# Kernel tuning notes

Measured on AMD Instinct MI355X. Metric: run time of the kernel, lower is better.

The kernel has to match this reference:

```python
import jax, jax.numpy as jnp
import numpy as np

B, S, DIM, H = 2, 2048, 1024, 16
HD = DIM // H  # 64


def setup_inputs() -> dict:
    key = jax.random.key(0)
    ks = jax.random.split(key, 7)
    sc = 1.0 / np.sqrt(DIM)
    gammas = jnp.asarray(1.0 - 2.0 ** (-5.0 - np.arange(H)), jnp.float32)  # RetNet per-head decay
    return {
        "q": jax.random.normal(ks[0], (B, S, DIM), jnp.float32),
        "k": jax.random.normal(ks[1], (B, S, DIM), jnp.float32),
        "v": jax.random.normal(ks[2], (B, S, DIM), jnp.float32),
        "W_in": jax.random.normal(ks[3], (DIM, DIM), jnp.float32) * sc,
        "b_in": jnp.zeros((DIM,), jnp.float32),
        "W_gate": jax.random.normal(ks[4], (DIM, DIM), jnp.float32) * sc,
        "b_gate": jnp.zeros((DIM,), jnp.float32),
        "W_out": jax.random.normal(ks[5], (DIM, DIM), jnp.float32) * sc,
        "b_out": jnp.zeros((DIM,), jnp.float32),
        "gammas": gammas,
    }


def _mamba(x, W_in, b_in, W_gate, b_gate, W_out, b_out):
    # Gated linear recurrence: h_t = a_t * h_{t-1} + u_t  (selective-scan style)
    u = x @ W_in + b_in          # [B,S,D]
    a = jax.nn.sigmoid(x @ W_gate + b_gate)  # [B,S,D] data-dependent decay gate

    def combine(c1, c2):
        a1, u1 = c1
        a2, u2 = c2
        return (a1 * a2, a2 * u1 + u2)

    _, h = jax.lax.associative_scan(combine, (a, u), axis=1)  # parallel scan over S
    return h @ W_out + b_out  # residual=False, dropout=0.0


def _retention(q, k, v, gammas):
    # Per-head decay-masked attention: out = ((Q K^T / sqrt(hd)) * D) V,
    # D[h,n,m] = gamma_h^(n-m) for n>=m else 0 (causal decay kernel).
    def split(x):
        return x.reshape(B, S, H, HD).transpose(0, 2, 1, 3)  # [B,H,S,HD]

    qh, kh, vh = split(q), split(k), split(v)
    idx = jnp.arange(S)
    diff = idx[:, None] - idx[None, :]                        # [S,S]
    expnt = jnp.maximum(diff, 0).astype(jnp.float32)
    D = jnp.where(diff >= 0, gammas[:, None, None] ** expnt, 0.0)  # [H,S,S]
    scores = jnp.einsum("bhnd,bhmd->bhnm", qh, kh) / np.sqrt(HD)
    out = jnp.einsum("bhnm,bhmd->bhnd", scores * D[None], vh)
    return out.transpose(0, 2, 1, 3).reshape(B, S, DIM)


def reference(q, k, v, W_in, b_in, W_gate, b_gate, W_out, b_out, gammas):
    q_proj = _mamba(q, W_in, b_in, W_gate, b_gate, W_out, b_out)
    return _retention(q_proj, k, v, gammas)
```

## Files before the change

kernel.cpp:

```cpp
#include <hip/hip_runtime.h>
#include <math.h>

#define B_  2
#define S_  2048
#define D_  1024
#define H_  16
#define HD_ 64
#define M_  (B_*S_)

typedef unsigned short ushort_t;
typedef unsigned int   uint_t;
typedef __attribute__((ext_vector_type(8))) short bf16x8;
typedef __attribute__((ext_vector_type(4))) float f32x4;

__device__ __forceinline__ ushort_t f2bf(float f) {
    uint_t u = __builtin_bit_cast(uint_t, f);
    u += 0x7FFFu + ((u >> 16) & 1u);
    return (ushort_t)(u >> 16);
}
__device__ __forceinline__ float bf2f(ushort_t h) {
    uint_t u = (uint_t)h << 16;
    return __builtin_bit_cast(float, u);
}
__device__ __forceinline__ uint_t pkt(float lo, float hi) {
    return __builtin_amdgcn_perm(__builtin_bit_cast(uint_t, hi),
                                 __builtin_bit_cast(uint_t, lo), 0x07060302u);
}
__device__ __forceinline__ void dma16(const ushort_t* g, ushort_t* l) {
    __builtin_amdgcn_global_load_lds(
        (const __attribute__((address_space(1))) uint_t*)g,
        (__attribute__((address_space(3))) uint_t*)l, 16, 0, 0);
}
__device__ __forceinline__ bf16x8 fragr(const ushort_t* base, int row, int chunk) {
    return *(const bf16x8*)&base[row * 64 + (((chunk ^ (row & 7)) << 3))];
}

__global__ __launch_bounds__(256)
void prep(const float* __restrict__ W0, const float* __restrict__ W1,
          const float* __restrict__ W2, ushort_t* __restrict__ T0,
          ushort_t* __restrict__ T1, ushort_t* __restrict__ T2,
          const float* __restrict__ X, ushort_t* __restrict__ Y) {
    const int bx = blockIdx.x;
    if (bx >= 3072) {
        const int i = ((bx - 3072) * 256 + threadIdx.x) * 4;
        float4 x = *(const float4*)(X + i);
        *(ushort4*)(Y + i) = make_ushort4(f2bf(x.x), f2bf(x.y), f2bf(x.z), f2bf(x.w));
        return;
    }
    __shared__ float T[32][36];
    const int z = bx >> 10;
    const float*  W  = (z == 0) ? W0 : (z == 1) ? W1 : W2;
    ushort_t*     WT = (z == 0) ? T0 : (z == 1) ? T1 : T2;
    const int kt = bx & 31, nt = (bx >> 5) & 31;
    const int t = threadIdx.x;
    const int rr = t >> 3, cc = (t & 7) * 4;
    float4 w4 = *(const float4*)(W + (size_t)(kt * 32 + rr) * D_ + nt * 32 + cc);
    T[rr][cc + 0] = w4.x; T[rr][cc + 1] = w4.y; T[rr][cc + 2] = w4.z; T[rr][cc + 3] = w4.w;
    __syncthreads();
    ushort_t o[4];
    #pragma unroll
    for (int j = 0; j < 4; ++j) o[j] = f2bf(T[cc + j][rr]);
    *(ushort4*)(WT + (size_t)(nt * 32 + rr) * D_ + kt * 32 + cc) =
        make_ushort4(o[0], o[1], o[2], o[3]);
}

__global__ __launch_bounds__(256)
void gemm_dual_kv(const ushort_t* __restrict__ A, const ushort_t* __restrict__ BTi,
                  const ushort_t* __restrict__ BTg, const float* __restrict__ bi,
                  const float* __restrict__ bg, uint_t* __restrict__ PH,
                  float* __restrict__ cA, float* __restrict__ cU,
                  const float* __restrict__ K, const float* __restrict__ V,
                  const float* __restrict__ gammas, ushort_t* __restrict__ Kb,
                  ushort_t* __restrict__ VT, float* __restrict__ Gg) {
    __shared__ ushort_t smem[32768];
    const int tid = threadIdx.x;
    const int w = tid >> 6, lane = tid & 63, quad = lane >> 4, l15 = lane & 15;

    if (blockIdx.x >= 512) {
        ushort_t* Tv = smem;
        ushort_t* Tk = smem + 64 * 72;
        const int idx = blockIdx.x - 512;
        const int mt = idx & 31, h = (idx >> 5) & 15, b = idx >> 9;
        const int m0 = mt * 64;
        const int r = tid >> 2, c0 = (tid & 3) * 16;
        const float lg = log2f(gammas[h]);
        const float gm = exp2f(-(float)r * lg);
        {
            const float* src = K + ((size_t)(b * S_ + m0 + r)) * D_ + h * HD_ + c0;
            ushort_t kb[16];
            #pragma unroll
            for (int j4 = 0; j4 < 4; ++j4) {
                float4 x = *(const float4*)(src + j4 * 4);
                kb[j4 * 4 + 0] = f2bf(x.x); kb[j4 * 4 + 1] = f2bf(x.y);
                kb[j4 * 4 + 2] = f2bf(x.z); kb[j4 * 4 + 3] = f2bf(x.w);
            }
            ushort_t* dst = Kb + ((size_t)(b * S_ + m0 + r)) * D_ + h * HD_ + c0;
            *(uint4*)(dst + 0) = *(const uint4*)&kb[0];
            *(uint4*)(dst + 8) = *(const uint4*)&kb[8];
            #pragma unroll
            for (int j = 0; j < 16; ++j) Tk[(c0 + j) * 72 + r] = kb[j];
        }
        {
            const float* src = V + ((size_t)(b * S_ + m0 + r)) * D_ + h * HD_ + c0;
            #pragma unroll
            for (int j4 = 0; j4 < 4; ++j4) {
                float4 x = *(const float4*)(src + j4 * 4);
                Tv[(c0 + j4 * 4 + 0) * 72 + r] = f2bf(x.x * gm);
                Tv[(c0 + j4 * 4 + 1) * 72 + r] = f2bf(x.y * gm);
                Tv[(c0 + j4 * 4 + 2) * 72 + r] = f2bf(x.z * gm);
                Tv[(c0 + j4 * 4 + 3) * 72 + r] = f2bf(x.w * gm);
            }
        }
        __syncthreads();
        {
            ushort_t* dst = VT + ((size_t)((b * H_ + h) * HD_ + r)) * S_ + m0 + c0;
            *(uint4*)(dst + 0) = *(const uint4*)&Tv[r * 72 + c0 + 0];
            *(uint4*)(dst + 8) = *(const uint4*)&Tv[r * 72 + c0 + 8];
        }
        bf16x8 af0 = *(const bf16x8*)&Tv[(w * 16 + l15) * 72 + quad * 8];
        bf16x8 af1 = *(const bf16x8*)&Tv[(w * 16 + l15) * 72 + 32 + quad * 8];
        float* gout = Gg + ((size_t)((b * H_ + h) * 32 + mt)) * 4096;
        #pragma unroll
        for (int kt2 = 0; kt2 < 4; ++kt2) {
            bf16x8 bf0 = *(const bf16x8*)&Tk[(kt2 * 16 + l15) * 72 + quad * 8];
            bf16x8 bf1 = *(const bf16x8*)&Tk[(kt2 * 16 + l15) * 72 + 32 + quad * 8];
            f32x4 g = {};
            g = __builtin_amdgcn_mfma_f32_16x16x32_bf16(af0, bf0, g, 0, 0, 0);
            g = __builtin_amdgcn_mfma_f32_16x16x32_bf16(af1, bf1, g, 0, 0, 0);
            #pragma unroll
            for (int reg = 0; reg < 4; ++reg)
                gout[(w * 16 + quad * 4 + reg) * 64 + kt2 * 16 + l15] = g[reg];
        }
        return;
    }

    const int swz = (blockIdx.x & 7) * 64 + (blockIdx.x >> 3);
    const int n0 = (swz & 15) * 64, m0 = (swz >> 4) * 128;
    const int wr = (w >> 1) * 64, wc = (w & 1) * 32;
    const int l8 = lane & 7, lr8 = lane >> 3;

    f32x4 acc_i[4][2] = {};
    f32x4 acc_g[4][2] = {};

    auto stage = [&](int k0, int bufo) {
        #pragma unroll
        for (int t = 0; t < 4; ++t) {
            const int row = w * 32 + t * 8 + lr8;
            const int gc = ((l8 ^ (row & 7)) << 3);
            dma16(A + (size_t)(m0 + row) * D_ + k0 + gc, &smem[bufo + row * 64 + l8 * 8]);
        }
        #pragma unroll
        for (int t = 0; t < 2; ++t) {
            const int row = w * 16 + t * 8 + lr8;
            const int gc = ((l8 ^ (row & 7)) << 3);
            dma16(BTi + (size_t)(n0 + row) * D_ + k0 + gc, &smem[bufo + 8192 + row * 64 + l8 * 8]);
            dma16(BTg + (size_t)(n0 + row) * D_ + k0 + gc, &smem[bufo + 12288 + row * 64 + l8 * 8]);
        }
    };

    stage(0, 0);
    __syncthreads();
    for (int t = 0; t < 16; ++t) {
        const int bufo = (t & 1) * 16384;
        if (t < 15) stage((t + 1) * 64, 16384 - bufo);
        const ushort_t* As = smem + bufo;
        const ushort_t* Bi = smem + bufo + 8192;
        const ushort_t* Bg = smem + bufo + 12288;
        #pragma unroll
        for (int kk = 0; kk < 2; ++kk) {
            bf16x8 af[4], bfi[2], bfg[2];
            #pragma unroll
            for (int i = 0; i < 4; ++i)
                af[i] = fragr(As, wr + 16 * i + l15, kk * 4 + quad);
            #pragma unroll
            for (int j = 0; j < 2; ++j) {
                bfi[j] = fragr(Bi, wc + 16 * j + l15, kk * 4 + quad);
                bfg[j] = fragr(Bg, wc + 16 * j + l15, kk * 4 + quad);
            }
            #pragma unroll
            for (int i = 0; i < 4; ++i)
                #pragma unroll
                for (int j = 0; j < 2; ++j) {
                    acc_i[i][j] = __builtin_amdgcn_mfma_f32_16x16x32_bf16(
                        af[i], bfi[j], acc_i[i][j], 0, 0, 0);
                    acc_g[i][j] = __builtin_amdgcn_mfma_f32_16x16x32_bf16(
                        af[i], bfg[j], acc_g[i][j], 0, 0, 0);
                }
        }
        __syncthreads();
    }

    ushort_t* Us = smem;
    ushort_t* Gu = smem + 8448;
    #pragma unroll
    for (int j = 0; j < 2; ++j) {
        const int n = wc + 16 * j + l15;
        const float bbi = bi[n0 + n], bbg = bg[n0 + n];
        #pragma unroll
        for (int i = 0; i < 4; ++i) {
            #pragma unroll
            for (int r = 0; r < 4; ++r) {
                const int m = wr + 16 * i + quad * 4 + r;
                Us[m * 66 + n] = f2bf(acc_i[i][j][r] + bbi);
                float g = 1.0f / (1.0f + __expf(-(acc_g[i][j][r] + bbg)));
                Gu[m * 66 + n] = (ushort_t)__float2uint_rn(g * 65535.0f);
            }
        }
    }
    __syncthreads();

    const int nl = tid & 63, c = tid >> 6;
    const int gmb = m0 + c * 32;
    const size_t gbase = (size_t)gmb * D_ + n0 + nl;
    float Aa = 1.0f, hh = 0.0f;
    #pragma unroll 4
    for (int j = 0; j < 32; ++j) {
        const float g = (float)Gu[(c * 32 + j) * 66 + nl] * (1.0f / 65535.0f);
        const float u = bf2f(Us[(c * 32 + j) * 66 + nl]);
        Aa *= g;
        hh = fmaf(g, hh, u);
        PH[gbase + (size_t)j * D_] = (uint_t)f2bf(Aa) | ((uint_t)f2bf(hh) << 16);
    }
    const int bb = gmb >> 11;
    const int ch = (gmb & 2047) >> 5;
    const int ci = ((bb * 64 + ch) << 10) + n0 + nl;
    cA[ci] = Aa;
    cU[ci] = hh;
}

__global__ __launch_bounds__(256)
void mid_scan(const float* __restrict__ Gg, const float* __restrict__ gammas,
              ushort_t* __restrict__ Sb, const float* __restrict__ cA,
              const float* __restrict__ cU, float* __restrict__ cIn) {
    const int bi = blockIdx.x;
    if (bi < 128) {
        const int sl = bi & 3, h = (bi >> 2) & 15, b = bi >> 6;
        const float g64 = exp2f(64.0f * log2f(gammas[h]));
        const int r = threadIdx.x >> 4;
        const int cb = (threadIdx.x & 15) * 4;
        const size_t base = ((size_t)((b * H_ + h) * 32)) * 4096 + (sl * 16 + r) * 64 + cb;
        float4 S = make_float4(0.f, 0.f, 0.f, 0.f);
        for (int c = 0; c < 32; ++c) {
            ushort4 sb;
            sb.x = f2bf(S.x); sb.y = f2bf(S.y); sb.z = f2bf(S.z); sb.w = f2bf(S.w);
            *(ushort4*)(Sb + base + (size_t)c * 4096) = sb;
            float4 G = *(const float4*)(Gg + base + (size_t)c * 4096);
            S.x = g64 * (S.x + G.x); S.y = g64 * (S.y + G.y);
            S.z = g64 * (S.z + G.z); S.w = g64 * (S.w + G.w);
        }
        return;
    }
    const int t = (bi - 128) * 256 + threadIdx.x;
    const int d = t & 1023, b = t >> 10;
    float h = 0.0f;
    for (int c0 = 0; c0 < 64; c0 += 16) {
        float Av[16], Uv[16];
        #pragma unroll
        for (int j = 0; j < 16; ++j) {
            const int idx = ((b * 64 + c0 + j) << 10) + d;
            Av[j] = cA[idx]; Uv[j] = cU[idx];
        }
        #pragma unroll
        for (int j = 0; j < 16; ++j) {
            cIn[((b * 64 + c0 + j) << 10) + d] = h;
            h = fmaf(Av[j], h, Uv[j]);
        }
    }
}

__global__ __launch_bounds__(256)
void scan_fix(const uint_t* __restrict__ PH, const float* __restrict__ cIn,
              ushort_t* __restrict__ hout) {
    const int i = (blockIdx.x * 256 + threadIdx.x) * 4;
    const int m = i >> 10, d = i & 1023;
    const int b = m >> 11, ch = (m & 2047) >> 5;
    uint4 ph = *(const uint4*)(PH + i);
    float4 ci = *(const float4*)(cIn + ((b * 64 + ch) << 10) + d);
    ushort4 o;
    o.x = f2bf(fmaf(ci.x, bf2f((ushort_t)(ph.x & 0xFFFF)), bf2f((ushort_t)(ph.x >> 16))));
    o.y = f2bf(fmaf(ci.y, bf2f((ushort_t)(ph.y & 0xFFFF)), bf2f((ushort_t)(ph.y >> 16))));
    o.z = f2bf(fmaf(ci.z, bf2f((ushort_t)(ph.z & 0xFFFF)), bf2f((ushort_t)(ph.z >> 16))));
    o.w = f2bf(fmaf(ci.w, bf2f((ushort_t)(ph.w & 0xFFFF)), bf2f((ushort_t)(ph.w >> 16))));
    *(ushort4*)(hout + i) = o;
}

__global__ __launch_bounds__(256)
void gemm_out_ret(const ushort_t* __restrict__ A, const ushort_t* __restrict__ BT,
                  const float* __restrict__ bias, const ushort_t* __restrict__ Kb,
                  const ushort_t* __restrict__ VT, const ushort_t* __restrict__ Sb,
                  const float* __restrict__ gammas, float* __restrict__ Out) {
    __shared__ ushort_t smem[24576];
    const int tid = threadIdx.x;
    const int flat = blockIdx.x + (blockIdx.y << 4);
    const int swz = (flat & 7) * 64 + (flat >> 3);
    const int h = swz & 15;
    const int n0 = h * 64, m0 = (swz >> 4) * 128;
    const int w = tid >> 6, lane = tid & 63, quad = lane >> 4, l15 = lane & 15;
    const int wr = (w >> 1) * 64, wc = (w & 1) * 32;
    const int l8 = lane & 7, lr8 = lane >> 3;

    ushort_t* Qs = smem;
    ushort_t* Ks = smem + 8192;
    ushort_t* Vt = smem + 12288;
    ushort_t* Ss = smem + 16384;
    ushort_t* Ps = smem + 20480;

    auto stageK = [&](int sc) {
        const int mrow = m0 + sc * 64;
        const size_t bS2 = (size_t)(mrow >> 11) * S_;
        const int s0r = mrow & 2047;
        #pragma unroll
        for (int t2 = 0; t2 < 2; ++t2) {
            const int row = w * 16 + t2 * 8 + lr8;
            const int gc = ((l8 ^ (row & 7)) << 3);
            dma16(Kb + (bS2 + s0r + row) * D_ + h * HD_ + gc, &Ks[row * 64 + l8 * 8]);
        }
    };
    auto stageV = [&](int sc) {
        const int mrow = m0 + sc * 64;
        const size_t vrow0 = (size_t)(((mrow >> 11) * H_ + h) * HD_);
        const int s0r = mrow & 2047;
        #pragma unroll
        for (int t2 = 0; t2 < 2; ++t2) {
            const int row = w * 16 + t2 * 8 + lr8;
            const int gc = ((l8 ^ (row & 7)) << 3);
            dma16(VT + (vrow0 + row) * S_ + s0r + gc, &Vt[row * 64 + l8 * 8]);
        }
    };
    auto stageS = [&](int sc) {
        const int mrow = m0 + sc * 64;
        const size_t sbase = ((size_t)(((mrow >> 11) * H_ + h) * 32 + ((mrow & 2047) >> 6))) * 4096;
        #pragma unroll
        for (int t2 = 0; t2 < 2; ++t2) {
            const int row = w * 16 + t2 * 8 + lr8;
            const int gc = ((l8 ^ (row & 7)) << 3);
            dma16(Sb + sbase + (size_t)row * 64 + gc, &Ss[row * 64 + l8 * 8]);
        }
    };

    f32x4 acc[4][2] = {};

    auto stage = [&](int k0, int bufo) {
        #pragma unroll
        for (int t = 0; t < 4; ++t) {
            const int row = w * 32 + t * 8 + lr8;
            const int gc = ((l8 ^ (row & 7)) << 3);
            dma16(A + (size_t)(m0 + row) * D_ + k0 + gc, &smem[bufo + row * 64 + l8 * 8]);
        }
        #pragma unroll
        for (int t = 0; t < 2; ++t) {
            const int row = w * 16 + t * 8 + lr8;
            const int gc = ((l8 ^ (row & 7)) << 3);
            dma16(BT + (size_t)(n0 + row) * D_ + k0 + gc, &smem[bufo + 8192 + row * 64 + l8 * 8]);
        }
    };

    stage(0, 0);
    __syncthreads();
    for (int t = 0; t < 16; ++t) {
        const int bufo = (t & 1) * 12288;
        if (t < 15) stage((t + 1) * 64, 12288 - bufo);
        if (t == 15) stageK(0);
        const ushort_t* As = smem + bufo;
        const ushort_t* Bs = smem + bufo + 8192;
        #pragma unroll
        for (int kk = 0; kk < 2; ++kk) {
            bf16x8 af[4], bf[2];
            #pragma unroll
            for (int i = 0; i < 4; ++i)
                af[i] = fragr(As, wr + 16 * i + l15, kk * 4 + quad);
            #pragma unroll
            for (int j = 0; j < 2; ++j)
                bf[j] = fragr(Bs, wc + 16 * j + l15, kk * 4 + quad);
            #pragma unroll
            for (int i = 0; i < 4; ++i)
                #pragma unroll
                for (int j = 0; j < 2; ++j)
                    acc[i][j] = __builtin_amdgcn_mfma_f32_16x16x32_bf16(
                        af[i], bf[j], acc[i][j], 0, 0, 0);
        }
        __syncthreads();
    }

    stageV(0);
    stageS(0);

    #pragma unroll
    for (int j = 0; j < 2; ++j) {
        const int n = wc + 16 * j + l15;
        const float bb = bias[n0 + n];
        #pragma unroll
        for (int i = 0; i < 4; ++i)
            #pragma unroll
            for (int r = 0; r < 4; ++r) {
                const int m = wr + 16 * i + quad * 4 + r;
                Qs[m * 64 + (((n >> 3) ^ (m & 7)) << 3) + (n & 7)] =
                    f2bf((acc[i][j][r] + bb) * 0.125f);
            }
    }

    const float lg = log2f(gammas[h]);
    const int nl = w * 16 + l15;

    for (int sc = 0; sc < 2; ++sc) {
        __syncthreads();
        const int mrow = m0 + sc * 64;
        const size_t bS = (size_t)(mrow >> 11) * S_;
        const int s0 = mrow & 2047;
        const ushort_t* Qsub = Qs + sc * 64 * 64;

        bf16x8 qf0 = fragr(Qsub, nl, quad);
        bf16x8 qf1 = fragr(Qsub, nl, 4 + quad);

        f32x4 o[4] = {};
        #pragma unroll
        for (int ct = 0; ct < 4; ++ct) {
            bf16x8 sf0 = fragr(Ss, ct * 16 + l15, quad);
            bf16x8 sf1 = fragr(Ss, ct * 16 + l15, 4 + quad);
            o[ct] = __builtin_amdgcn_mfma_f32_16x16x32_bf16(sf0, qf0, o[ct], 0, 0, 0);
            o[ct] = __builtin_amdgcn_mfma_f32_16x16x32_bf16(sf1, qf1, o[ct], 0, 0, 0);
        }
        uint2 pw[4];
        #pragma unroll
        for (int mt2 = 0; mt2 < 4; ++mt2) {
            bf16x8 kf0 = fragr(Ks, mt2 * 16 + l15, quad);
            bf16x8 kf1 = fragr(Ks, mt2 * 16 + l15, 4 + quad);
            f32x4 s = {};
            s = __builtin_amdgcn_mfma_f32_16x16x32_bf16(kf0, qf0, s, 0, 0, 0);
            s = __builtin_amdgcn_mfma_f32_16x16x32_bf16(kf1, qf1, s, 0, 0, 0);
            const int mbase = mt2 * 16 + quad * 4;
            #pragma unroll
            for (int r = 0; r < 4; ++r)
                if (nl < mbase + r) s[r] = 0.0f;
            pw[mt2].x = pkt(s[0], s[1]); pw[mt2].y = pkt(s[2], s[3]);
        }
        __syncthreads();
        if (sc == 0) { stageK(1); stageS(1); }
        #pragma unroll
        for (int mt2 = 0; mt2 < 4; ++mt2) {
            const int mbase = mt2 * 16 + quad * 4;
            const int chunk = mbase >> 3;
            *(uint2*)&Ps[nl * 64 + ((chunk ^ (nl & 7)) << 3) + (mbase & 7)] = pw[mt2];
        }
        bf16x8 pf0 = fragr(Ps, nl, quad);
        bf16x8 pf1 = fragr(Ps, nl, 4 + quad);
        #pragma unroll
        for (int ct = 0; ct < 4; ++ct) {
            bf16x8 vf0 = fragr(Vt, ct * 16 + l15, quad);
            bf16x8 vf1 = fragr(Vt, ct * 16 + l15, 4 + quad);
            o[ct] = __builtin_amdgcn_mfma_f32_16x16x32_bf16(vf0, pf0, o[ct], 0, 0, 0);
            o[ct] = __builtin_amdgcn_mfma_f32_16x16x32_bf16(vf1, pf1, o[ct], 0, 0, 0);
        }

        const float esc = exp2f((float)nl * lg);
        const size_t ob = (bS + s0 + nl) * D_ + h * HD_;
        #pragma unroll
        for (int ct = 0; ct < 4; ++ct) {
            f32x4 t = o[ct] * esc;
            *(f32x4*)(Out + ob + ct * 16 + quad * 4) = t;
        }
        __syncthreads();
        if (sc == 0) stageV(1);
    }
}

extern "C" void kernel_launch(void* const* d_in, const int* in_sizes, int n_in,
                              void* d_out, int out_size, void* d_ws, size_t ws_size,
                              hipStream_t stream) {
    const float* q      = (const float*)d_in[0];
    const float* k      = (const float*)d_in[1];
    const float* v      = (const float*)d_in[2];
    const float* W_in   = (const float*)d_in[3];
    const float* b_in   = (const float*)d_in[4];
    const float* W_gate = (const float*)d_in[5];
    const float* b_gate = (const float*)d_in[6];
    const float* W_out  = (const float*)d_in[7];
    const float* b_out  = (const float*)d_in[8];
    const float* gammas = (const float*)d_in[9];
    float* out = (float*)d_out;

    char* ws = (char*)d_ws;
    const size_t MB = 1024 * 1024;
    uint_t*   PH      = (uint_t*)(ws);
    ushort_t* h_bf    = (ushort_t*)(ws + 24 * MB);
    ushort_t* q_bf    = (ushort_t*)(ws + 32 * MB);
    ushort_t* WT_in   = (ushort_t*)(ws + 40 * MB);
    ushort_t* WT_gate = (ushort_t*)(ws + 42 * MB);
    ushort_t* WT_out  = (ushort_t*)(ws + 44 * MB);
    float*    cA      = (float*)(ws + 46 * MB);
    float*    cU      = (float*)(ws + 46 * MB + 512 * 1024);
    float*    cIn     = (float*)(ws + 47 * MB);
    ushort_t* k_bf    = (ushort_t*)(ws + 48 * MB);
    ushort_t* VT      = (ushort_t*)(ws + 56 * MB);
    float*    Gg      = (float*)(ws + 64 * MB);
    ushort_t* Sb      = (ushort_t*)(ws + 80 * MB);

    prep<<<3072 + (M_ * D_) / (256 * 4), 256, 0, stream>>>(
        W_in, W_gate, W_out, WT_in, WT_gate, WT_out, q, q_bf);

    gemm_dual_kv<<<512 + 1024, 256, 0, stream>>>(
        q_bf, WT_in, WT_gate, b_in, b_gate, PH, cA, cU,
        k, v, gammas, k_bf, VT, Gg);

    mid_scan<<<136, 256, 0, stream>>>(Gg, gammas, Sb, cA, cU, cIn);
    scan_fix<<<(M_ * D_) / 1024, 256, 0, stream>>>(PH, cIn, h_bf);

    gemm_out_ret<<<dim3(H_, M_ / 128), 256, 0, stream>>>(
        h_bf, WT_out, b_out, k_bf, VT, Sb, gammas, out);
}
```

Measured before the change: 174.4 us.

## Fuse scan fixup into output GEMM A-tile load and widen mid_scan grid

```diff
diff --git a/kernel.cpp b/kernel.cpp
--- a/kernel.cpp
+++ b/kernel.cpp
@@ -233,24 +233,22 @@
               ushort_t* __restrict__ Sb, const float* __restrict__ cA,
               const float* __restrict__ cU, float* __restrict__ cIn) {
     const int bi = blockIdx.x;
-    if (bi < 128) {
-        const int sl = bi & 3, h = (bi >> 2) & 15, b = bi >> 6;
+    if (bi < 512) {
+        const int bh = bi >> 4;
+        const int h = bh & 15;
+        const int e = (bi & 15) * 256 + threadIdx.x;
         const float g64 = exp2f(64.0f * log2f(gammas[h]));
-        const int r = threadIdx.x >> 4;
-        const int cb = (threadIdx.x & 15) * 4;
-        const size_t base = ((size_t)((b * H_ + h) * 32)) * 4096 + (sl * 16 + r) * 64 + cb;
-        float4 S = make_float4(0.f, 0.f, 0.f, 0.f);
+        const size_t base = (size_t)bh * 32 * 4096 + e;
+        float S = 0.0f;
+        #pragma unroll
         for (int c = 0; c < 32; ++c) {
-            ushort4 sb;
-            sb.x = f2bf(S.x); sb.y = f2bf(S.y); sb.z = f2bf(S.z); sb.w = f2bf(S.w);
-            *(ushort4*)(Sb + base + (size_t)c * 4096) = sb;
-            float4 G = *(const float4*)(Gg + base + (size_t)c * 4096);
-            S.x = g64 * (S.x + G.x); S.y = g64 * (S.y + G.y);
-            S.z = g64 * (S.z + G.z); S.w = g64 * (S.w + G.w);
+            Sb[base + (size_t)c * 4096] = f2bf(S);
+            const float G = Gg[base + (size_t)c * 4096];
+            S = g64 * (S + G);
         }
         return;
     }
-    const int t = (bi - 128) * 256 + threadIdx.x;
+    const int t = (bi - 512) * 256 + threadIdx.x;
     const int d = t & 1023, b = t >> 10;
     float h = 0.0f;
     for (int c0 = 0; c0 < 64; c0 += 16) {
@@ -269,26 +267,11 @@
 }
 
 __global__ __launch_bounds__(256)
-void scan_fix(const uint_t* __restrict__ PH, const float* __restrict__ cIn,
-              ushort_t* __restrict__ hout) {
-    const int i = (blockIdx.x * 256 + threadIdx.x) * 4;
-    const int m = i >> 10, d = i & 1023;
-    const int b = m >> 11, ch = (m & 2047) >> 5;
-    uint4 ph = *(const uint4*)(PH + i);
-    float4 ci = *(const float4*)(cIn + ((b * 64 + ch) << 10) + d);
-    ushort4 o;
-    o.x = f2bf(fmaf(ci.x, bf2f((ushort_t)(ph.x & 0xFFFF)), bf2f((ushort_t)(ph.x >> 16))));
-    o.y = f2bf(fmaf(ci.y, bf2f((ushort_t)(ph.y & 0xFFFF)), bf2f((ushort_t)(ph.y >> 16))));
-    o.z = f2bf(fmaf(ci.z, bf2f((ushort_t)(ph.z & 0xFFFF)), bf2f((ushort_t)(ph.z >> 16))));
-    o.w = f2bf(fmaf(ci.w, bf2f((ushort_t)(ph.w & 0xFFFF)), bf2f((ushort_t)(ph.w >> 16))));
-    *(ushort4*)(hout + i) = o;
-}
-
-__global__ __launch_bounds__(256)
-void gemm_out_ret(const ushort_t* __restrict__ A, const ushort_t* __restrict__ BT,
-                  const float* __restrict__ bias, const ushort_t* __restrict__ Kb,
-                  const ushort_t* __restrict__ VT, const ushort_t* __restrict__ Sb,
-                  const float* __restrict__ gammas, float* __restrict__ Out) {
+void gemm_out_ret(const uint_t* __restrict__ PH, const float* __restrict__ cIn,
+                  const ushort_t* __restrict__ BT, const float* __restrict__ bias,
+                  const ushort_t* __restrict__ Kb, const ushort_t* __restrict__ VT,
+                  const ushort_t* __restrict__ Sb, const float* __restrict__ gammas,
+                  float* __restrict__ Out) {
     __shared__ ushort_t smem[24576];
     const int tid = threadIdx.x;
     const int flat = blockIdx.x + (blockIdx.y << 4);
@@ -345,7 +328,25 @@
         for (int t = 0; t < 4; ++t) {
             const int row = w * 32 + t * 8 + lr8;
             const int gc = ((l8 ^ (row & 7)) << 3);
-            dma16(A + (size_t)(m0 + row) * D_ + k0 + gc, &smem[bufo + row * 64 + l8 * 8]);
+            const int m = m0 + row;
+            const int bb = m >> 11;
+            const int ch = (m & 2047) >> 5;
+            const uint_t* phs = PH + (size_t)m * D_ + k0 + gc;
+            const float* cis = cIn + (((bb * 64 + ch) << 10) + k0 + gc);
+            uint4 ph0 = *(const uint4*)(phs + 0);
+            uint4 ph1 = *(const uint4*)(phs + 4);
+            float4 ci0 = *(const float4*)(cis + 0);
+            float4 ci1 = *(const float4*)(cis + 4);
+            ushort_t hv[8];
+            hv[0] = f2bf(fmaf(ci0.x, bf2f((ushort_t)(ph0.x & 0xFFFF)), bf2f((ushort_t)(ph0.x >> 16))));
+            hv[1] = f2bf(fmaf(ci0.y, bf2f((ushort_t)(ph0.y & 0xFFFF)), bf2f((ushort_t)(ph0.y >> 16))));
+            hv[2] = f2bf(fmaf(ci0.z, bf2f((ushort_t)(ph0.z & 0xFFFF)), bf2f((ushort_t)(ph0.z >> 16))));
+            hv[3] = f2bf(fmaf(ci0.w, bf2f((ushort_t)(ph0.w & 0xFFFF)), bf2f((ushort_t)(ph0.w >> 16))));
+            hv[4] = f2bf(fmaf(ci1.x, bf2f((ushort_t)(ph1.x & 0xFFFF)), bf2f((ushort_t)(ph1.x >> 16))));
+            hv[5] = f2bf(fmaf(ci1.y, bf2f((ushort_t)(ph1.y & 0xFFFF)), bf2f((ushort_t)(ph1.y >> 16))));
+            hv[6] = f2bf(fmaf(ci1.z, bf2f((ushort_t)(ph1.z & 0xFFFF)), bf2f((ushort_t)(ph1.z >> 16))));
+            hv[7] = f2bf(fmaf(ci1.w, bf2f((ushort_t)(ph1.w & 0xFFFF)), bf2f((ushort_t)(ph1.w >> 16))));
+            *(uint4*)&smem[bufo + row * 64 + l8 * 8] = *(const uint4*)&hv[0];
         }
         #pragma unroll
         for (int t = 0; t < 2; ++t) {
@@ -482,7 +483,6 @@
     char* ws = (char*)d_ws;
     const size_t MB = 1024 * 1024;
     uint_t*   PH      = (uint_t*)(ws);
-    ushort_t* h_bf    = (ushort_t*)(ws + 24 * MB);
     ushort_t* q_bf    = (ushort_t*)(ws + 32 * MB);
     ushort_t* WT_in   = (ushort_t*)(ws + 40 * MB);
     ushort_t* WT_gate = (ushort_t*)(ws + 42 * MB);
@@ -502,9 +502,8 @@
         q_bf, WT_in, WT_gate, b_in, b_gate, PH, cA, cU,
         k, v, gammas, k_bf, VT, Gg);
 
-    mid_scan<<<136, 256, 0, stream>>>(Gg, gammas, Sb, cA, cU, cIn);
-    scan_fix<<<(M_ * D_) / 1024, 256, 0, stream>>>(PH, cIn, h_bf);
+    mid_scan<<<520, 256, 0, stream>>>(Gg, gammas, Sb, cA, cU, cIn);
 
     gemm_out_ret<<<dim3(H_, M_ / 128), 256, 0, stream>>>(
-        h_bf, WT_out, b_out, k_bf, VT, Sb, gammas, out);
-}
+        PH, cIn, WT_out, b_out, k_bf, VT, Sb, gammas, out);
+}
```

New measurement: 191.5 us. +9.8%, slower.
